# Performance work log

Hardware: AMD Instinct MI355X
Metric: run time of the kernel (lower is better)

## Reference

```python
import jax, jax.numpy as jnp
import numpy as np

B, T, IN, H3, OUT = 64, 512, 512, 512, 256  # hidden_size=1536 -> h_third=512


def setup_inputs() -> dict:
    key = jax.random.key(0)
    ks = jax.random.split(key, 14)
    w = lambda k, i, o: jax.random.normal(k, (i, o), jnp.float32) * 0.02
    b = lambda k, o: jax.random.normal(k, (o,), jnp.float32) * 0.01
    return {
        "x": jax.random.normal(ks[0], (B, T, IN), jnp.float32),
        "Ws": w(ks[1], IN, H3), "bs": b(ks[2], H3),
        "Wi": w(ks[3], H3, H3), "bi": b(ks[4], H3),
        "Wc": w(ks[5], H3, H3), "bc": b(ks[6], H3),
        "Wm": w(ks[7], H3, OUT), "bm": b(ks[8], OUT),
        "Wir": w(ks[9], H3, H3), "bir": b(ks[10], H3),
        "Wcr": w(ks[11], H3, H3), "bcr": b(ks[12], H3),
        "tau_s": jnp.full((H3,), 5.0, jnp.float32),
        "tau_i": jnp.full((H3,), 10.0, jnp.float32),
        "tau_c": jnp.full((H3,), 20.0, jnp.float32),
    }


def reference(x, Ws, bs, Wi, bi, Wc, bc, Wm, bm, Wir, bir, Wcr, bcr, tau_s, tau_i, tau_c):
    Bv = x.shape[0]
    inv_s, inv_i, inv_c = 1.0 / tau_s, 1.0 / tau_i, 1.0 / tau_c
    h0 = (jnp.zeros((Bv, H3), x.dtype),) * 3

    def step(carry, x_t):
        hs, hi, hc = carry
        hs = (1 - inv_s) * hs + inv_s * jnp.tanh(x_t @ Ws + bs)
        hi = (1 - inv_i) * hi + inv_i * jnp.tanh(hs @ Wi + bi + hi @ Wir + bir)
        hc = (1 - inv_c) * hc + inv_c * jnp.tanh(hi @ Wc + bc + hc @ Wcr + bcr)
        out = hc @ Wm + bm
        return (hs, hi, hc), out

    _, outs = jax.lax.scan(step, h0, jnp.swapaxes(x, 0, 1))  # [T,B,OUT]
    return jnp.swapaxes(outs, 0, 1)  # [B,T,OUT]
```

## Files before the change

kernel.cpp:

```cpp
#include <hip/hip_runtime.h>
#include <cmath>

constexpr int Bv  = 64;
constexpr int T   = 512;
constexpr int H   = 512;
constexpr int OUTD = 256;
constexpr int M   = Bv * T;

__global__ __launch_bounds__(256) void gemm_bias_act(
    const float* __restrict__ A, const float* __restrict__ W,
    const float* __restrict__ b1, const float* __restrict__ b2,
    float* __restrict__ C, int N, int do_tanh)
{
    constexpr int K = 512;
    __shared__ float As[16][132];
    __shared__ float Bs[16][128];

    const int tid  = threadIdx.x;
    const int row0 = blockIdx.x * 128;
    const int col0 = blockIdx.y * 128;
    const int tx = tid & 15, ty = tid >> 4;

    const int ar = tid >> 2;
    const int ak = (tid & 3) * 4;
    const int bk = tid >> 4;
    const int bn = (tid & 15) * 8;

    float acc[8][8] = {};

    const float* Aptr = A + (size_t)(row0 + ar) * K + ak;
    const float* Wptr = W + (size_t)bk * N + col0 + bn;

    for (int k0 = 0; k0 < K; k0 += 16) {
        const float4 a0 = *(const float4*)(Aptr + k0);
        const float4 a1 = *(const float4*)(Aptr + (size_t)64 * K + k0);
        const float4 bv0 = *(const float4*)(Wptr + (size_t)k0 * N);
        const float4 bv1 = *(const float4*)(Wptr + (size_t)k0 * N + 4);
        As[ak + 0][ar] = a0.x;  As[ak + 1][ar] = a0.y;
        As[ak + 2][ar] = a0.z;  As[ak + 3][ar] = a0.w;
        As[ak + 0][ar + 64] = a1.x;  As[ak + 1][ar + 64] = a1.y;
        As[ak + 2][ar + 64] = a1.z;  As[ak + 3][ar + 64] = a1.w;
        *(float4*)&Bs[bk][bn]     = bv0;
        *(float4*)&Bs[bk][bn + 4] = bv1;
        __syncthreads();
        #pragma unroll
        for (int k = 0; k < 16; ++k) {
            const float4 xa = *(const float4*)&As[k][ty * 8];
            const float4 xb = *(const float4*)&As[k][ty * 8 + 4];
            const float4 ya = *(const float4*)&Bs[k][tx * 8];
            const float4 yb = *(const float4*)&Bs[k][tx * 8 + 4];
            const float a8[8] = {xa.x, xa.y, xa.z, xa.w, xb.x, xb.y, xb.z, xb.w};
            const float b8[8] = {ya.x, ya.y, ya.z, ya.w, yb.x, yb.y, yb.z, yb.w};
            #pragma unroll
            for (int i = 0; i < 8; ++i)
                #pragma unroll
                for (int j = 0; j < 8; ++j)
                    acc[i][j] = fmaf(a8[i], b8[j], acc[i][j]);
        }
        __syncthreads();
    }

    float4 bias0 = *(const float4*)&b1[col0 + tx * 8];
    float4 bias1 = *(const float4*)&b1[col0 + tx * 8 + 4];
    if (b2 != nullptr) {
        const float4 e0 = *(const float4*)&b2[col0 + tx * 8];
        const float4 e1 = *(const float4*)&b2[col0 + tx * 8 + 4];
        bias0.x += e0.x; bias0.y += e0.y; bias0.z += e0.z; bias0.w += e0.w;
        bias1.x += e1.x; bias1.y += e1.y; bias1.z += e1.z; bias1.w += e1.w;
    }
    #pragma unroll
    for (int i = 0; i < 8; ++i) {
        float4 v0, v1;
        v0.x = acc[i][0] + bias0.x;  v0.y = acc[i][1] + bias0.y;
        v0.z = acc[i][2] + bias0.z;  v0.w = acc[i][3] + bias0.w;
        v1.x = acc[i][4] + bias1.x;  v1.y = acc[i][5] + bias1.y;
        v1.z = acc[i][6] + bias1.z;  v1.w = acc[i][7] + bias1.w;
        if (do_tanh) {
            v0.x = tanhf(v0.x); v0.y = tanhf(v0.y); v0.z = tanhf(v0.z); v0.w = tanhf(v0.w);
            v1.x = tanhf(v1.x); v1.y = tanhf(v1.y); v1.z = tanhf(v1.z); v1.w = tanhf(v1.w);
        }
        float* crow = &C[(size_t)(row0 + ty * 8 + i) * N + col0 + tx * 8];
        *(float4*)crow       = v0;
        *(float4*)(crow + 4) = v1;
    }
}

__global__ __launch_bounds__(256) void scan_hs_kernel(
    float* __restrict__ buf, const float* __restrict__ tau)
{
    const int h  = blockIdx.x * 256 + threadIdx.x;
    const int b0 = blockIdx.y * 2;
    const float inv = 1.0f / tau[h];
    const float am  = 1.0f - inv;
    float s0 = 0.f, s1 = 0.f;
    const size_t bs_ = (size_t)T * H;
    const size_t i0 = (size_t)b0 * bs_ + h;
    #pragma unroll 4
    for (int t = 0; t < T; ++t) {
        const size_t o = i0 + (size_t)t * H;
        const float x0 = buf[o];
        const float x1 = buf[o + bs_];
        s0 = am * s0 + inv * x0;
        s1 = am * s1 + inv * x1;
        buf[o]       = s0;
        buf[o + bs_] = s1;
    }
}

#define WLOAD(i) float4 w##i = *(const float4*)&Wr[(size_t)(k0 + (i)) * H + j0];

#define PIN4(a,b,c,d) asm volatile("" :                                   \
    "+v"(a.x), "+v"(a.y), "+v"(a.z), "+v"(a.w),                           \
    "+v"(b.x), "+v"(b.y), "+v"(b.z), "+v"(b.w),                           \
    "+v"(c.x), "+v"(c.y), "+v"(c.z), "+v"(c.w),                           \
    "+v"(d.x), "+v"(d.y), "+v"(d.z), "+v"(d.w));

#define FMAG(wa, wb, wc, wd)                              \
    acc.x = fmaf(h4.x, wa.x, acc.x);                      \
    acc.y = fmaf(h4.x, wa.y, acc.y);                      \
    acc.z = fmaf(h4.x, wa.z, acc.z);                      \
    acc.w = fmaf(h4.x, wa.w, acc.w);                      \
    acc.x = fmaf(h4.y, wb.x, acc.x);                      \
    acc.y = fmaf(h4.y, wb.y, acc.y);                      \
    acc.z = fmaf(h4.y, wb.z, acc.z);                      \
    acc.w = fmaf(h4.y, wb.w, acc.w);                      \
    acc.x = fmaf(h4.z, wc.x, acc.x);                      \
    acc.y = fmaf(h4.z, wc.y, acc.y);                      \
    acc.z = fmaf(h4.z, wc.z, acc.z);                      \
    acc.w = fmaf(h4.z, wc.w, acc.w);                      \
    acc.x = fmaf(h4.w, wd.x, acc.x);                      \
    acc.y = fmaf(h4.w, wd.y, acc.y);                      \
    acc.z = fmaf(h4.w, wd.z, acc.z);                      \
    acc.w = fmaf(h4.w, wd.w, acc.w);

__global__ __launch_bounds__(512)
__attribute__((amdgpu_waves_per_eu(2, 2)))
void recur_kernel(
    const float* __restrict__ U, float* __restrict__ Hout,
    const float* __restrict__ Wr, const float* __restrict__ tau,
    unsigned long long* __restrict__ xbuf)
{
    __shared__ float h_lds[H];
    __shared__ float accb[16][128];

    const int tid = threadIdx.x;
    const int bid = blockIdx.x;
    const int x = bid & 7, q = bid >> 3;
    const int r = (q >> 2) * 8 + x;
    const int p = q & 3;
    const int p128 = p * 128;

    const int cg = tid & 31;
    const int s  = tid >> 5;
    const int k0 = s * 32;
    const int j0 = p128 + cg * 4;

    WLOAD(0)  WLOAD(1)  WLOAD(2)  WLOAD(3)
    WLOAD(4)  WLOAD(5)  WLOAD(6)  WLOAD(7)
    WLOAD(8)  WLOAD(9)  WLOAD(10) WLOAD(11)
    WLOAD(12) WLOAD(13) WLOAD(14) WLOAD(15)
    WLOAD(16) WLOAD(17) WLOAD(18) WLOAD(19)
    WLOAD(20) WLOAD(21) WLOAD(22) WLOAD(23)
    WLOAD(24) WLOAD(25) WLOAD(26) WLOAD(27)
    WLOAD(28) WLOAD(29) WLOAD(30) WLOAD(31)

    float inv = 0.f, am = 0.f, h_reg = 0.f;
    const float* Urow = nullptr;
    float*       Hrow = nullptr;
    if (tid < 128) {
        inv = 1.0f / tau[p128 + tid];
        am  = 1.0f - inv;
        Urow = U    + (size_t)r * T * H + p128 + tid;
        Hrow = Hout + (size_t)r * T * H + p128 + tid;
    }
    unsigned long long* __restrict__ xrow = xbuf + (size_t)r * 2 * H;

    h_lds[tid] = 0.0f;
    __syncthreads();

    float uval = 0.f, unext = 0.f;
    if (tid < 128) uval = Urow[0];

    for (int t = 0; t < T; ++t) {
        PIN4(w0,  w1,  w2,  w3)   PIN4(w4,  w5,  w6,  w7)
        PIN4(w8,  w9,  w10, w11)  PIN4(w12, w13, w14, w15)
        PIN4(w16, w17, w18, w19)  PIN4(w20, w21, w22, w23)
        PIN4(w24, w25, w26, w27)  PIN4(w28, w29, w30, w31)

        if (tid < 128 && t + 1 < T) unext = Urow[(size_t)(t + 1) * H];

        float4 acc = make_float4(0.f, 0.f, 0.f, 0.f);
        float4 h4;
        h4 = *(const float4*)&h_lds[k0 +  0]; FMAG(w0,  w1,  w2,  w3)
        h4 = *(const float4*)&h_lds[k0 +  4]; FMAG(w4,  w5,  w6,  w7)
        h4 = *(const float4*)&h_lds[k0 +  8]; FMAG(w8,  w9,  w10, w11)
        h4 = *(const float4*)&h_lds[k0 + 12]; FMAG(w12, w13, w14, w15)
        h4 = *(const float4*)&h_lds[k0 + 16]; FMAG(w16, w17, w18, w19)
        h4 = *(const float4*)&h_lds[k0 + 20]; FMAG(w20, w21, w22, w23)
        h4 = *(const float4*)&h_lds[k0 + 24]; FMAG(w24, w25, w26, w27)
        h4 = *(const float4*)&h_lds[k0 + 28]; FMAG(w28, w29, w30, w31)
        *(float4*)&accb[s][cg * 4] = acc;
        __syncthreads();

        if (tid < 128) {
            float red = 0.f;
            #pragma unroll
            for (int ss = 0; ss < 16; ++ss) red += accb[ss][tid];
            const float a = red + uval;
            const float hnew = am * h_reg + inv * tanhf(a);
            h_reg = hnew;
            if (t + 1 < T) {
                const unsigned long long pv =
                    ((unsigned long long)(unsigned)(t + 1) << 32) |
                    (unsigned long long)__float_as_uint(hnew);
                __hip_atomic_store(&xrow[(size_t)(t & 1) * H + p128 + tid], pv,
                                   __ATOMIC_RELAXED, __HIP_MEMORY_SCOPE_AGENT);
            }
            Hrow[(size_t)t * H] = hnew;
            h_lds[p128 + tid] = hnew;
        }

        if (t + 1 < T) {
            if (tid >= 128) {
                const int e = (p128 + tid) & 511;
                unsigned long long* slot = &xrow[(size_t)(t & 1) * H + e];
                unsigned long long v;
                do {
                    v = __hip_atomic_load(slot, __ATOMIC_RELAXED,
                                          __HIP_MEMORY_SCOPE_AGENT);
                } while ((int)(v >> 32) != t + 1);
                h_lds[e] = __uint_as_float((unsigned)v);
            }
            uval = unext;
            __syncthreads();
        }
    }
}

extern "C" void kernel_launch(void* const* d_in, const int* in_sizes, int n_in,
                              void* d_out, int out_size, void* d_ws, size_t ws_size,
                              hipStream_t stream)
{
    const float* x     = (const float*)d_in[0];
    const float* Ws    = (const float*)d_in[1];
    const float* bs    = (const float*)d_in[2];
    const float* Wi    = (const float*)d_in[3];
    const float* bi    = (const float*)d_in[4];
    const float* Wc    = (const float*)d_in[5];
    const float* bc    = (const float*)d_in[6];
    const float* Wm    = (const float*)d_in[7];
    const float* bm    = (const float*)d_in[8];
    const float* Wir   = (const float*)d_in[9];
    const float* bir   = (const float*)d_in[10];
    const float* Wcr   = (const float*)d_in[11];
    const float* bcr   = (const float*)d_in[12];
    const float* tau_s = (const float*)d_in[13];
    const float* tau_i = (const float*)d_in[14];
    const float* tau_c = (const float*)d_in[15];
    float* out = (float*)d_out;

    float* bufA = (float*)d_ws;
    float* bufB = bufA + (size_t)M * H;
    unsigned long long* xbuf1 = (unsigned long long*)d_out;
    unsigned long long* xbuf2 = xbuf1 + (size_t)Bv * 2 * H;

    const dim3 blk(256);

    gemm_bias_act<<<dim3(M / 128, H / 128), blk, 0, stream>>>(x, Ws, bs, nullptr, bufA, H, 1);
    scan_hs_kernel<<<dim3(H / 256, Bv / 2), blk, 0, stream>>>(bufA, tau_s);
    gemm_bias_act<<<dim3(M / 128, H / 128), blk, 0, stream>>>(bufA, Wi, bi, bir, bufB, H, 0);
    recur_kernel<<<dim3(256), dim3(512), 0, stream>>>(bufB, bufA, Wir, tau_i, xbuf1);
    gemm_bias_act<<<dim3(M / 128, H / 128), blk, 0, stream>>>(bufA, Wc, bc, bcr, bufB, H, 0);
    recur_kernel<<<dim3(256), dim3(512), 0, stream>>>(bufB, bufA, Wcr, tau_c, xbuf2);
    gemm_bias_act<<<dim3(M / 128, OUTD / 128), blk, 0, stream>>>(bufA, Wm, bm, nullptr, out, OUTD, 0);
}
```

Baseline: 2.492 ms.

## Replace FP32 SIMT GEMMs with split-bf16 MFMA GEMMs

Replaces the scalar FMA tiled GEMM with a matrix-core kernel that splits each fp32 operand into high and low bf16 parts and accumulates three-to-four bf16 MFMA products to approximate fp32 accuracy. Tiles are staged in LDS as bf16 with an XOR swizzle on the weight tile to avoid bank conflicts. This is meant to move the large feed-forward GEMMs onto matrix cores. In exchange it adds conversion work per tile, does 4x the MFMA count, and writes output with scalar stores.

After: 2.104 ms. 15.6% less time.

```diff
diff --git a/kernel.cpp b/kernel.cpp
--- a/kernel.cpp
+++ b/kernel.cpp
@@ -7,81 +7,130 @@
 constexpr int OUTD = 256;
 constexpr int M   = Bv * T;
 
-__global__ __launch_bounds__(256) void gemm_bias_act(
+typedef __attribute__((ext_vector_type(8))) short short8;
+typedef __attribute__((ext_vector_type(4))) short short4v;
+typedef __attribute__((ext_vector_type(4))) float f32x4;
+
+__device__ __forceinline__ unsigned short bf16_rn(float f) {
+    unsigned u = __float_as_uint(f);
+    return (unsigned short)((u + 0x7FFFu + ((u >> 16) & 1u)) >> 16);
+}
+__device__ __forceinline__ void split2(float f, unsigned short& h, unsigned short& l) {
+    h = bf16_rn(f);
+    l = bf16_rn(f - __uint_as_float(((unsigned)h) << 16));
+}
+
+__global__ __launch_bounds__(256) void gemm_mfma(
     const float* __restrict__ A, const float* __restrict__ W,
     const float* __restrict__ b1, const float* __restrict__ b2,
     float* __restrict__ C, int N, int do_tanh)
 {
     constexpr int K = 512;
-    __shared__ float As[16][132];
-    __shared__ float Bs[16][128];
+    constexpr int P = 40;
+    __shared__ unsigned short Ah[128][P], Al[128][P];
+    __shared__ unsigned short Wh[128][P], Wl[128][P];
 
     const int tid  = threadIdx.x;
+    const int lane = tid & 63;
+    const int wid  = tid >> 6;
+    const int wm   = wid >> 1, wn = wid & 1;
     const int row0 = blockIdx.x * 128;
     const int col0 = blockIdx.y * 128;
-    const int tx = tid & 15, ty = tid >> 4;
-
-    const int ar = tid >> 2;
-    const int ak = (tid & 3) * 4;
-    const int bk = tid >> 4;
-    const int bn = (tid & 15) * 8;
-
-    float acc[8][8] = {};
-
-    const float* Aptr = A + (size_t)(row0 + ar) * K + ak;
-    const float* Wptr = W + (size_t)bk * N + col0 + bn;
-
-    for (int k0 = 0; k0 < K; k0 += 16) {
-        const float4 a0 = *(const float4*)(Aptr + k0);
-        const float4 a1 = *(const float4*)(Aptr + (size_t)64 * K + k0);
-        const float4 bv0 = *(const float4*)(Wptr + (size_t)k0 * N);
-        const float4 bv1 = *(const float4*)(Wptr + (size_t)k0 * N + 4);
-        As[ak + 0][ar] = a0.x;  As[ak + 1][ar] = a0.y;
-        As[ak + 2][ar] = a0.z;  As[ak + 3][ar] = a0.w;
-        As[ak + 0][ar + 64] = a1.x;  As[ak + 1][ar + 64] = a1.y;
-        As[ak + 2][ar + 64] = a1.z;  As[ak + 3][ar + 64] = a1.w;
-        *(float4*)&Bs[bk][bn]     = bv0;
-        *(float4*)&Bs[bk][bn + 4] = bv1;
+
+    const int l15 = lane & 15;
+    const int l4  = lane >> 4;
+    const int kb  = l4 * 8;
+
+    const int am  = tid >> 1;
+    const int akq = (tid & 1) * 16;
+    const int wk4 = (tid >> 5) * 4;
+    const int wn4 = (tid & 31) * 4;
+
+    f32x4 acc[4][4];
+    #pragma unroll
+    for (int i = 0; i < 4; ++i)
+        #pragma unroll
+        for (int j = 0; j < 4; ++j) {
+            f32x4 z = {0.f, 0.f, 0.f, 0.f};
+            acc[i][j] = z;
+        }
+
+    for (int k0 = 0; k0 < K; k0 += 32) {
+        {
+            const float* ap = A + (size_t)(row0 + am) * K + k0 + akq;
+            #pragma unroll
+            for (int c = 0; c < 4; ++c) {
+                const float4 v = *(const float4*)(ap + c * 4);
+                unsigned short h0, l0, h1, l1, h2, l2, h3, l3;
+                split2(v.x, h0, l0); split2(v.y, h1, l1);
+                split2(v.z, h2, l2); split2(v.w, h3, l3);
+                short4v sh = {(short)h0, (short)h1, (short)h2, (short)h3};
+                short4v sl = {(short)l0, (short)l1, (short)l2, (short)l3};
+                *(short4v*)&Ah[am][akq + c * 4] = sh;
+                *(short4v*)&Al[am][akq + c * 4] = sl;
+            }
+        }
+        {
+            float arr[4][4];
+            #pragma unroll
+            for (int i = 0; i < 4; ++i) {
+                const float4 v = *(const float4*)(W + (size_t)(k0 + wk4 + i) * N + col0 + wn4);
+                arr[i][0] = v.x; arr[i][1] = v.y; arr[i][2] = v.z; arr[i][3] = v.w;
+            }
+            #pragma unroll
+            for (int j = 0; j < 4; ++j) {
+                const int n = wn4 + j;
+                const int kbase = wk4 ^ (((n >> 2) & 3) << 3);
+                unsigned short h0, l0, h1, l1, h2, l2, h3, l3;
+                split2(arr[0][j], h0, l0); split2(arr[1][j], h1, l1);
+                split2(arr[2][j], h2, l2); split2(arr[3][j], h3, l3);
+                short4v sh = {(short)h0, (short)h1, (short)h2, (short)h3};
+                short4v sl = {(short)l0, (short)l1, (short)l2, (short)l3};
+                *(short4v*)&Wh[n][kbase] = sh;
+                *(short4v*)&Wl[n][kbase] = sl;
+            }
+        }
         __syncthreads();
+
+        short8 ahf[4], alf[4];
         #pragma unroll
-        for (int k = 0; k < 16; ++k) {
-            const float4 xa = *(const float4*)&As[k][ty * 8];
-            const float4 xb = *(const float4*)&As[k][ty * 8 + 4];
-            const float4 ya = *(const float4*)&Bs[k][tx * 8];
-            const float4 yb = *(const float4*)&Bs[k][tx * 8 + 4];
-            const float a8[8] = {xa.x, xa.y, xa.z, xa.w, xb.x, xb.y, xb.z, xb.w};
-            const float b8[8] = {ya.x, ya.y, ya.z, ya.w, yb.x, yb.y, yb.z, yb.w};
-            #pragma unroll
-            for (int i = 0; i < 8; ++i)
-                #pragma unroll
-                for (int j = 0; j < 8; ++j)
-                    acc[i][j] = fmaf(a8[i], b8[j], acc[i][j]);
+        for (int fi = 0; fi < 4; ++fi) {
+            const int r = wm * 64 + fi * 16 + l15;
+            ahf[fi] = *(const short8*)&Ah[r][kb];
+            alf[fi] = *(const short8*)&Al[r][kb];
+        }
+        #pragma unroll
+        for (int fj = 0; fj < 4; ++fj) {
+            const int n  = wn * 64 + fj * 16 + l15;
+            const int kk = kb ^ (((n >> 2) & 3) << 3);
+            const short8 bh = *(const short8*)&Wh[n][kk];
+            const short8 bl = *(const short8*)&Wl[n][kk];
+            #pragma unroll
+            for (int fi = 0; fi < 4; ++fi) {
+                acc[fi][fj] = __builtin_amdgcn_mfma_f32_16x16x32_bf16(ahf[fi], bh, acc[fi][fj], 0, 0, 0);
+                acc[fi][fj] = __builtin_amdgcn_mfma_f32_16x16x32_bf16(alf[fi], bh, acc[fi][fj], 0, 0, 0);
+                acc[fi][fj] = __builtin_amdgcn_mfma_f32_16x16x32_bf16(ahf[fi], bl, acc[fi][fj], 0, 0, 0);
+                acc[fi][fj] = __builtin_amdgcn_mfma_f32_16x16x32_bf16(alf[fi], bl, acc[fi][fj], 0, 0, 0);
+            }
         }
         __syncthreads();
     }
 
-    float4 bias0 = *(const float4*)&b1[col0 + tx * 8];
-    float4 bias1 = *(const float4*)&b1[col0 + tx * 8 + 4];
-    if (b2 != nullptr) {
-        const float4 e0 = *(const float4*)&b2[col0 + tx * 8];
-        const float4 e1 = *(const float4*)&b2[col0 + tx * 8 + 4];
-        bias0.x += e0.x; bias0.y += e0.y; bias0.z += e0.z; bias0.w += e0.w;
-        bias1.x += e1.x; bias1.y += e1.y; bias1.z += e1.z; bias1.w += e1.w;
-    }
     #pragma unroll
-    for (int i = 0; i < 8; ++i) {
-        float4 v0, v1;
-        v0.x = acc[i][0] + bias0.x;  v0.y = acc[i][1] + bias0.y;
-        v0.z = acc[i][2] + bias0.z;  v0.w = acc[i][3] + bias0.w;
-        v1.x = acc[i][4] + bias1.x;  v1.y = acc[i][5] + bias1.y;
-        v1.z = acc[i][6] + bias1.z;  v1.w = acc[i][7] + bias1.w;
-        if (do_tanh) {
-            v0.x = tanhf(v0.x); v0.y = tanhf(v0.y); v0.z = tanhf(v0.z); v0.w = tanhf(v0.w);
-            v1.x = tanhf(v1.x); v1.y = tanhf(v1.y); v1.z = tanhf(v1.z); v1.w = tanhf(v1.w);
-        }
-        float* crow = &C[(size_t)(row0 + ty * 8 + i) * N + col0 + tx * 8];
-        *(float4*)crow       = v0;
-        *(float4*)(crow + 4) = v1;
+    for (int fj = 0; fj < 4; ++fj) {
+        const int col = col0 + wn * 64 + fj * 16 + l15;
+        float bias = b1[col];
+        if (b2 != nullptr) bias += b2[col];
+        #pragma unroll
+        for (int fi = 0; fi < 4; ++fi) {
+            const int rbase = row0 + wm * 64 + fi * 16 + l4 * 4;
+            #pragma unroll
+            for (int j = 0; j < 4; ++j) {
+                float v = acc[fi][fj][j] + bias;
+                if (do_tanh) v = tanhf(v);
+                C[(size_t)(rbase + j) * N + col] = v;
+            }
+        }
     }
 }
 
@@ -266,11 +315,11 @@
 
     const dim3 blk(256);
 
-    gemm_bias_act<<<dim3(M / 128, H / 128), blk, 0, stream>>>(x, Ws, bs, nullptr, bufA, H, 1);
+    gemm_mfma<<<dim3(M / 128, H / 128), blk, 0, stream>>>(x, Ws, bs, nullptr, bufA, H, 1);
     scan_hs_kernel<<<dim3(H / 256, Bv / 2), blk, 0, stream>>>(bufA, tau_s);
-    gemm_bias_act<<<dim3(M / 128, H / 128), blk, 0, stream>>>(bufA, Wi, bi, bir, bufB, H, 0);
+    gemm_mfma<<<dim3(M / 128, H / 128), blk, 0, stream>>>(bufA, Wi, bi, bir, bufB, H, 0);
     recur_kernel<<<dim3(256), dim3(512), 0, stream>>>(bufB, bufA, Wir, tau_i, xbuf1);
-    gemm_bias_act<<<dim3(M / 128, H / 128), blk, 0, stream>>>(bufA, Wc, bc, bcr, bufB, H, 0);
+    gemm_mfma<<<dim3(M / 128, H / 128), blk, 0, stream>>>(bufA, Wc, bc, bcr, bufB, H, 0);
     recur_kernel<<<dim3(256), dim3(512), 0, stream>>>(bufB, bufA, Wcr, tau_c, xbuf2);
-    gemm_bias_act<<<dim3(M / 128, OUTD / 128), blk, 0, stream>>>(bufA, Wm, bm, nullptr, out, OUTD, 0);
-}
+    gemm_mfma<<<dim3(M / 128, OUTD / 128), blk, 0, stream>>>(bufA, Wm, bm, nullptr, out, OUTD, 0);
+}
```
